# Kernel tuning notes

Measured on AMD Instinct MI355X. Metric: run time of the kernel, lower is better.

## Reference

```python
import jax, jax.numpy as jnp
import numpy as np


def _binarize(x):
    # sign binarization to {-1, +1}; sign(0) -> +1
    return jnp.where(x >= 0, 1.0, -1.0).astype(x.dtype)


def setup_inputs() -> dict:
    key = jax.random.key(0)
    kx, kw, kb = jax.random.split(key, 3)
    C_in, C_out, K = 128, 128, 3
    x = jax.random.normal(kx, (32, C_in, 112, 112), dtype=jnp.float32)
    # conv weight [C_out, C_in, K, K], kaiming-ish scale
    W = jax.random.normal(kw, (C_out, C_in, K, K), dtype=jnp.float32) * (1.0 / np.sqrt(C_in * K * K))
    b = jax.random.normal(kb, (C_out,), dtype=jnp.float32) * 0.01
    return {"x": x, "W": W, "b": b}


def reference(x, W, b):
    # BinConv: binarize activations, binarize weights, then standard conv2d
    xb = _binarize(x)                # [N, C_in, H, W] in {-1, +1}
    Wb = _binarize(W)                # [C_out, C_in, K, K] in {-1, +1}
    out = jax.lax.conv_general_dilated(
        xb, Wb,
        window_strides=(1, 1),
        padding=((1, 1), (1, 1)),
        rhs_dilation=(1, 1),
        dimension_numbers=("NCHW", "OIHW", "NCHW"),
    )
    return out + b[None, :, None, None]
```

## Files before the change

kernel.cpp:

```cpp
#include <hip/hip_runtime.h>
#include <stdint.h>

#define Hdim 112
#define Wdim 112
#define CIN  128
#define COUT 128
#define NB   32
#define HW   (Hdim*Wdim)
#define HALO_W 114
#define HALO_PX (4*HALO_W)
#define SLOT_STRIDE (HALO_PX*16)


typedef int   v4i __attribute__((ext_vector_type(4)));
typedef int  v16i __attribute__((ext_vector_type(16)));
typedef float v4f __attribute__((ext_vector_type(4)));

__global__ void pack_w_i8(const float* __restrict__ W, char* __restrict__ Wi8) {
    int t = blockIdx.x * blockDim.x + threadIdx.x;
    if (t >= COUT * 9) return;
    int co = t / 9, tap = t % 9;
    const float* wp = W + (size_t)co * CIN * 9 + tap;
    uint32_t* dst = (uint32_t*)(Wi8 + ((size_t)tap * COUT + co) * CIN);
    #pragma unroll
    for (int c4 = 0; c4 < 32; c4++) {
        uint32_t word = 0;
        #pragma unroll
        for (int j = 0; j < 4; j++) {
            uint32_t neg = __float_as_uint(wp[(size_t)(c4 * 4 + j) * 9]) >> 31;
            word |= (neg ? 0xFFu : 0x01u) << (8 * j);
        }
        dst[c4] = word;
    }
}

__global__ __launch_bounds__(256) void pack_x_kernel(const float* __restrict__ x,
                                                     uint4* __restrict__ pkx) {
    int gid = blockIdx.x * blockDim.x + threadIdx.x;
    int n = gid / (HW / 4);
    int p = (gid - n * (HW / 4)) * 4;
    const float* xp = x + (size_t)n * CIN * HW + p;
    uint32_t m[4][4] = {{0,0,0,0},{0,0,0,0},{0,0,0,0},{0,0,0,0}};
    #pragma unroll
    for (int c = 0; c < CIN; c++) {
        v4f v = __builtin_nontemporal_load(
            reinterpret_cast<const v4f*>(xp + (size_t)c * HW));
        int q = c >> 5, s = c & 31;
        m[0][q] |= (__float_as_uint(v.x) >> 31) << s;
        m[1][q] |= (__float_as_uint(v.y) >> 31) << s;
        m[2][q] |= (__float_as_uint(v.z) >> 31) << s;
        m[3][q] |= (__float_as_uint(v.w) >> 31) << s;
    }
    uint4* op = pkx + (size_t)n * HW + p;
    #pragma unroll
    for (int j = 0; j < 4; j++)
        op[j] = make_uint4(m[j][0], m[j][1], m[j][2], m[j][3]);
}

__device__ __forceinline__ uint32_t expand4(uint32_t b) {
    uint32_t s = ((b & 0xFu) * 0x00204081u) & 0x01010101u;
    return 0x01010101u ^ (s * 0xFEu);
}

__global__ __launch_bounds__(256, 2) void binconv_mfma(
    const uint4* __restrict__ pkx, const char* __restrict__ Wi8,
    const float* __restrict__ bias, float* __restrict__ out) {
    __shared__ char halo[8 * SLOT_STRIDE];

    int tid = threadIdx.x;
    int hy = blockIdx.x;
    int n  = blockIdx.y;
    int h0 = hy * 2;

    for (int i = tid; i < HALO_PX; i += 256) {
        int r = i / HALO_W, c = i - r * HALO_W;
        int h = h0 - 1 + r, w = c - 1;
        bool valid = (h >= 0) && (h < Hdim) && (w >= 0) && (w < Wdim);
        uint32_t keep = valid ? 0xFFFFFFFFu : 0u;
        int hc = min(max(h, 0), Hdim - 1);
        int wc = min(max(w, 0), Wdim - 1);
        uint4 bits = pkx[(size_t)n * HW + hc * Wdim + wc];
        uint32_t src[4] = {bits.x, bits.y, bits.z, bits.w};
        #pragma unroll
        for (int s = 0; s < 8; s++) {
            uint32_t q = src[s >> 1] >> ((s & 1) * 16);
            uint4 ov;
            ov.x = expand4(q)       & keep;
            ov.y = expand4(q >> 4)  & keep;
            ov.z = expand4(q >> 8)  & keep;
            ov.w = expand4(q >> 12) & keep;
            *reinterpret_cast<uint4*>(&halo[s * SLOT_STRIDE + i * 16]) = ov;
        }
    }

    int wid = tid >> 6, l = tid & 63;
    int al = l & 31, ah = l >> 5;
    int cobase = wid * 32;

    int hb[7];
    #pragma unroll
    for (int pt = 0; pt < 7; pt++) {
        int P = pt * 32 + al;
        int r = (P >= Wdim) ? 1 : 0;
        int w = P - r * Wdim;
        hb[pt] = (r * HALO_W + w) * 16 + ah * SLOT_STRIDE;
    }

    const char* wA = Wi8 + ((size_t)cobase + al) * CIN + ah * 16;

    v16i acc[7];
    #pragma unroll
    for (int pt = 0; pt < 7; pt++)
        #pragma unroll
        for (int i = 0; i < 16; i++) acc[pt][i] = 0;

    v4i A[4];
    #pragma unroll
    for (int kk = 0; kk < 4; kk++)
        A[kk] = *reinterpret_cast<const v4i*>(wA + kk * 32);

    __syncthreads();

    #pragma unroll
    for (int tap = 0; tap < 9; tap++) {
        v4i N[4];
        if (tap < 8) {
            const char* wt = wA + (size_t)(tap + 1) * COUT * CIN;
            #pragma unroll
            for (int kk = 0; kk < 4; kk++)
                N[kk] = *reinterpret_cast<const v4i*>(wt + kk * 32);
        }
        const int dy = tap / 3, dx = tap % 3;
        const int imm = (dy * HALO_W + dx) * 16;
        #pragma unroll
        for (int kk = 0; kk < 4; kk++) {
            const int simm = imm + kk * 2 * SLOT_STRIDE;
            v4i b[7];
            #pragma unroll
            for (int pt = 0; pt < 7; pt++)
                b[pt] = *reinterpret_cast<const v4i*>(&halo[hb[pt] + simm]);
            #pragma unroll
            for (int pt = 0; pt < 7; pt++)
                acc[pt] = __builtin_amdgcn_mfma_i32_32x32x32_i8(A[kk], b[pt], acc[pt], 0, 0, 0);
        }
        if (tap < 8) {
            #pragma unroll
            for (int kk = 0; kk < 4; kk++) A[kk] = N[kk];
        }
    }

    float* ob = out + (size_t)n * COUT * HW + (size_t)h0 * Wdim;
    #pragma unroll
    for (int reg = 0; reg < 16; reg++) {
        int co = cobase + (reg & 3) + ((reg >> 2) << 3) + (ah << 2);
        float bv = bias[co];
        float* op = ob + (size_t)co * HW + al;
        #pragma unroll
        for (int pt = 0; pt < 7; pt++)
            __builtin_nontemporal_store((float)acc[pt][reg] + bv, op + pt * 32);
    }
}

extern "C" void kernel_launch(void* const* d_in, const int* in_sizes, int n_in,
                              void* d_out, int out_size, void* d_ws, size_t ws_size,
                              hipStream_t stream) {
    const float* x = (const float*)d_in[0];
    const float* W = (const float*)d_in[1];
    const float* b = (const float*)d_in[2];
    float* out = (float*)d_out;
    char* ws = (char*)d_ws;
    char*  Wi8 = ws;
    uint4* pkx = (uint4*)(ws + 147456);

    pack_w_i8<<<dim3((COUT * 9 + 255) / 256), dim3(256), 0, stream>>>(W, Wi8);
    pack_x_kernel<<<dim3(NB * HW / 4 / 256), dim3(256), 0, stream>>>(x, pkx);
    binconv_mfma<<<dim3(Hdim / 2, NB), dim3(256), 0, stream>>>(pkx, Wi8, b, out);
}
```

Baseline: 126.9 us.

## Process two row-pairs per block with a rolling four-row halo ring buffer

Each block now computes four output rows instead of two. It keeps a 4-row ring buffer in LDS and restages only the two new halo rows between iterations, so the two overlapping rows are reused instead of reloaded and re-expanded. This halves the grid size and cuts redundant halo staging and pkx reads. The cost is extra barriers in the middle of the kernel and fewer blocks for latency hiding.

```diff
diff --git a/kernel.cpp b/kernel.cpp
--- a/kernel.cpp
+++ b/kernel.cpp
@@ -8,8 +8,9 @@
 #define NB   32
 #define HW   (Hdim*Wdim)
 #define HALO_W 114
-#define HALO_PX (4*HALO_W)
-#define SLOT_STRIDE (HALO_PX*16)
+#define ROWSTR (HALO_W*16)
+#define SLOT_STRIDE (4*ROWSTR)
+#define IT 2
 
 
 typedef int   v4i __attribute__((ext_vector_type(4)));
@@ -62,6 +63,27 @@
     return 0x01010101u ^ (s * 0xFEu);
 }
 
+__device__ __forceinline__ void stage_px(const uint4* __restrict__ pkx, char* halo,
+                                         int n, int h, int w, int ring, int c) {
+    bool valid = (h >= 0) && (h < Hdim) && (w >= 0) && (w < Wdim);
+    uint32_t keep = valid ? 0xFFFFFFFFu : 0u;
+    int hc = min(max(h, 0), Hdim - 1);
+    int wc = min(max(w, 0), Wdim - 1);
+    uint4 bits = pkx[(size_t)n * HW + hc * Wdim + wc];
+    uint32_t src[4] = {bits.x, bits.y, bits.z, bits.w};
+    unsigned base = (unsigned)(ring * ROWSTR + c * 16);
+    #pragma unroll
+    for (int sl = 0; sl < 8; sl++) {
+        uint32_t q = src[sl >> 1] >> ((sl & 1) * 16);
+        uint4 ov;
+        ov.x = expand4(q)       & keep;
+        ov.y = expand4(q >> 4)  & keep;
+        ov.z = expand4(q >> 8)  & keep;
+        ov.w = expand4(q >> 12) & keep;
+        *reinterpret_cast<uint4*>(&halo[sl * SLOT_STRIDE + base]) = ov;
+    }
+}
+
 __global__ __launch_bounds__(256, 2) void binconv_mfma(
     const uint4* __restrict__ pkx, const char* __restrict__ Wi8,
     const float* __restrict__ bias, float* __restrict__ out) {
@@ -70,94 +92,99 @@
     int tid = threadIdx.x;
     int hy = blockIdx.x;
     int n  = blockIdx.y;
-    int h0 = hy * 2;
-
-    for (int i = tid; i < HALO_PX; i += 256) {
+    int h0 = hy * (2 * IT);
+
+    for (int i = tid; i < 4 * HALO_W; i += 256) {
         int r = i / HALO_W, c = i - r * HALO_W;
-        int h = h0 - 1 + r, w = c - 1;
-        bool valid = (h >= 0) && (h < Hdim) && (w >= 0) && (w < Wdim);
-        uint32_t keep = valid ? 0xFFFFFFFFu : 0u;
-        int hc = min(max(h, 0), Hdim - 1);
-        int wc = min(max(w, 0), Wdim - 1);
-        uint4 bits = pkx[(size_t)n * HW + hc * Wdim + wc];
-        uint32_t src[4] = {bits.x, bits.y, bits.z, bits.w};
-        #pragma unroll
-        for (int s = 0; s < 8; s++) {
-            uint32_t q = src[s >> 1] >> ((s & 1) * 16);
-            uint4 ov;
-            ov.x = expand4(q)       & keep;
-            ov.y = expand4(q >> 4)  & keep;
-            ov.z = expand4(q >> 8)  & keep;
-            ov.w = expand4(q >> 12) & keep;
-            *reinterpret_cast<uint4*>(&halo[s * SLOT_STRIDE + i * 16]) = ov;
-        }
+        stage_px(pkx, halo, n, h0 - 1 + r, c - 1, r, c);
     }
 
     int wid = tid >> 6, l = tid & 63;
     int al = l & 31, ah = l >> 5;
     int cobase = wid * 32;
 
-    int hb[7];
+    int colb[7], rsel[7], wcol[7];
     #pragma unroll
     for (int pt = 0; pt < 7; pt++) {
         int P = pt * 32 + al;
-        int r = (P >= Wdim) ? 1 : 0;
-        int w = P - r * Wdim;
-        hb[pt] = (r * HALO_W + w) * 16 + ah * SLOT_STRIDE;
+        rsel[pt] = (P >= Wdim) ? 1 : 0;
+        wcol[pt] = P - rsel[pt] * Wdim;
+        colb[pt] = wcol[pt] * 16 + ah * SLOT_STRIDE;
     }
 
     const char* wA = Wi8 + ((size_t)cobase + al) * CIN + ah * 16;
-
-    v16i acc[7];
-    #pragma unroll
-    for (int pt = 0; pt < 7; pt++)
-        #pragma unroll
-        for (int i = 0; i < 16; i++) acc[pt][i] = 0;
-
-    v4i A[4];
-    #pragma unroll
-    for (int kk = 0; kk < 4; kk++)
-        A[kk] = *reinterpret_cast<const v4i*>(wA + kk * 32);
+    float* ob = out + (size_t)n * COUT * HW;
 
     __syncthreads();
 
     #pragma unroll
-    for (int tap = 0; tap < 9; tap++) {
-        v4i N[4];
-        if (tap < 8) {
-            const char* wt = wA + (size_t)(tap + 1) * COUT * CIN;
-            #pragma unroll
-            for (int kk = 0; kk < 4; kk++)
-                N[kk] = *reinterpret_cast<const v4i*>(wt + kk * 32);
-        }
-        const int dy = tap / 3, dx = tap % 3;
-        const int imm = (dy * HALO_W + dx) * 16;
-        #pragma unroll
-        for (int kk = 0; kk < 4; kk++) {
-            const int simm = imm + kk * 2 * SLOT_STRIDE;
-            v4i b[7];
+    for (int s = 0; s < IT; s++) {
+        const int hs = h0 + 2 * s;
+
+        v16i acc[7];
+        #pragma unroll
+        for (int pt = 0; pt < 7; pt++)
+            #pragma unroll
+            for (int i = 0; i < 16; i++) acc[pt][i] = 0;
+
+        v4i A[4];
+        #pragma unroll
+        for (int kk = 0; kk < 4; kk++)
+            A[kk] = *reinterpret_cast<const v4i*>(wA + kk * 32);
+
+        #pragma unroll
+        for (int tap = 0; tap < 9; tap++) {
+            v4i N[4];
+            if (tap < 8) {
+                const char* wt = wA + (size_t)(tap + 1) * COUT * CIN;
+                #pragma unroll
+                for (int kk = 0; kk < 4; kk++)
+                    N[kk] = *reinterpret_cast<const v4i*>(wt + kk * 32);
+            }
+            const int dy = tap / 3, dx = tap % 3;
+            int po[7];
             #pragma unroll
             for (int pt = 0; pt < 7; pt++)
-                b[pt] = *reinterpret_cast<const v4i*>(&halo[hb[pt] + simm]);
-            #pragma unroll
-            for (int pt = 0; pt < 7; pt++)
-                acc[pt] = __builtin_amdgcn_mfma_i32_32x32x32_i8(A[kk], b[pt], acc[pt], 0, 0, 0);
-        }
-        if (tap < 8) {
-            #pragma unroll
-            for (int kk = 0; kk < 4; kk++) A[kk] = N[kk];
-        }
-    }
-
-    float* ob = out + (size_t)n * COUT * HW + (size_t)h0 * Wdim;
-    #pragma unroll
-    for (int reg = 0; reg < 16; reg++) {
-        int co = cobase + (reg & 3) + ((reg >> 2) << 3) + (ah << 2);
-        float bv = bias[co];
-        float* op = ob + (size_t)co * HW + al;
-        #pragma unroll
-        for (int pt = 0; pt < 7; pt++)
-            __builtin_nontemporal_store((float)acc[pt][reg] + bv, op + pt * 32);
+                po[pt] = colb[pt] + (((2 * s + dy + rsel[pt]) & 3) * ROWSTR) + dx * 16;
+            #pragma unroll
+            for (int kk = 0; kk < 4; kk++) {
+                v4i b[7];
+                #pragma unroll
+                for (int pt = 0; pt < 7; pt++)
+                    b[pt] = *reinterpret_cast<const v4i*>(&halo[kk * 2 * SLOT_STRIDE + po[pt]]);
+                #pragma unroll
+                for (int pt = 0; pt < 7; pt++)
+                    acc[pt] = __builtin_amdgcn_mfma_i32_32x32x32_i8(A[kk], b[pt], acc[pt], 0, 0, 0);
+            }
+            if (tap < 8) {
+                #pragma unroll
+                for (int kk = 0; kk < 4; kk++) A[kk] = N[kk];
+            }
+        }
+
+        #pragma unroll
+        for (int reg = 0; reg < 16; reg++) {
+            int co = cobase + (reg & 3) + ((reg >> 2) << 3) + (ah << 2);
+            float bv = bias[co];
+            #pragma unroll
+            for (int pt = 0; pt < 7; pt++) {
+                size_t off = (size_t)co * HW + (size_t)(hs + rsel[pt]) * Wdim + wcol[pt];
+                __builtin_nontemporal_store((float)acc[pt][reg] + bv, &ob[off]);
+            }
+        }
+
+        if (s + 1 < IT) {
+            asm volatile("s_waitcnt lgkmcnt(0)" ::: "memory");
+            __builtin_amdgcn_s_barrier();
+            __builtin_amdgcn_sched_barrier(0);
+            for (int i = tid; i < 2 * HALO_W; i += 256) {
+                int r = i / HALO_W, c = i - r * HALO_W;
+                stage_px(pkx, halo, n, hs + 3 + r, c - 1, (2 * s + r) & 3, c);
+            }
+            asm volatile("s_waitcnt lgkmcnt(0)" ::: "memory");
+            __builtin_amdgcn_s_barrier();
+            __builtin_amdgcn_sched_barrier(0);
+        }
     }
 }
 
@@ -174,5 +201,5 @@
 
     pack_w_i8<<<dim3((COUT * 9 + 255) / 256), dim3(256), 0, stream>>>(W, Wi8);
     pack_x_kernel<<<dim3(NB * HW / 4 / 256), dim3(256), 0, stream>>>(x, pkx);
-    binconv_mfma<<<dim3(Hdim / 2, NB), dim3(256), 0, stream>>>(pkx, Wi8, b, out);
-}
+    binconv_mfma<<<dim3(Hdim / (2 * IT), NB), dim3(256), 0, stream>>>(pkx, Wi8, b, out);
+}
```

Measured after the change: 124.2 us (median of 4 runs). 1.02x faster.
